# Optimization experiments

Measured on AMD Instinct MI355X. Metric: run time of the kernel, lower is better.

Reference implementation:

```python
import jax, jax.numpy as jnp
import numpy as np

DIM_IN = 512
HIDDEN = 512
DIM_OUT = 512
BATCH = 256

def _n_tri(d):
    return (d * d + d) // 2

def _quad_expand(x):
    # x: [B, D] -> [B, D + (D^2+D)/2] with upper-triu (incl diag) pairwise products
    d = x.shape[1]
    iu0, iu1 = np.triu_indices(d)  # static indices
    x_sq = x[:, iu0] * x[:, iu1]  # [B, n_tri] -- avoids materializing full outer
    return jnp.concatenate([x, x_sq], axis=-1)

def setup_inputs() -> dict:
    key = jax.random.key(0)
    k = jax.random.split(key, 5)
    f0 = DIM_IN + _n_tri(DIM_IN)
    f1 = HIDDEN + _n_tri(HIDDEN)
    s0 = 1.0 / np.sqrt(f0)
    s1 = 1.0 / np.sqrt(f1)
    return {
        "x": jax.random.normal(k[0], (BATCH, DIM_IN), dtype=jnp.float32),
        "W0": jax.random.uniform(k[1], (HIDDEN, f0), dtype=jnp.float32, minval=-s0, maxval=s0),
        "b0": jax.random.uniform(k[2], (HIDDEN,), dtype=jnp.float32, minval=-s0, maxval=s0),
        "W1": jax.random.uniform(k[3], (DIM_OUT, f1), dtype=jnp.float32, minval=-s1, maxval=s1),
        "b1": jax.random.uniform(k[4], (DIM_OUT,), dtype=jnp.float32, minval=-s1, maxval=s1),
    }

def reference(x, W0, b0, W1, b1):
    h = _quad_expand(x) @ W0.T + b0  # [B, HIDDEN]
    out = _quad_expand(h) @ W1.T + b1  # [B, DIM_OUT]
    return out
```

## Files before the change

kernel.cpp:

```cpp
#include <hip/hip_runtime.h>

typedef short s16x4 __attribute__((ext_vector_type(4)));
typedef short s16x8 __attribute__((ext_vector_type(8)));
typedef float f32x4 __attribute__((ext_vector_type(4)));

#define DIM     512
#define BATCH   256
#define NTRI    131328
#define FDIM    131840
#define KBLOCKS 2060
#define BN      64
#define NTILES  8
#define CMAX    128

__device__ __forceinline__ unsigned short f2bf(float f) {
  __bf16 h = (__bf16)f;
  return __builtin_bit_cast(unsigned short, h);
}
__device__ __forceinline__ float bf2f(unsigned short s) {
  union { unsigned u; float f; } v; v.u = (unsigned)s << 16; return v.f;
}
__device__ __forceinline__ int swz(int m) { return (m ^ (m >> 2)) & 7; }

__global__ void build_table(unsigned* __restrict__ table) {
  int i = blockIdx.x;
  int base = i * DIM - (i * (i - 1)) / 2;
  int len = DIM - i;
  for (int t = threadIdx.x; t < len; t += blockDim.x)
    table[base + t] = ((unsigned)i << 16) | (unsigned)(i + t);
}

__global__ void transpose_x(const float* __restrict__ x, unsigned short* __restrict__ Xt) {
  int t = blockIdx.x * blockDim.x + threadIdx.x;
  int r = t & (BATCH - 1);
  int c = t >> 8;
  Xt[c * BATCH + r] = f2bf(x[r * DIM + c]);
}

__global__ __launch_bounds__(512, 4)
void qgemm(const unsigned* __restrict__ table,
           const unsigned short* __restrict__ Xt,
           const float* __restrict__ W,
           float* __restrict__ partial,
           int C)
{
  __shared__ unsigned short As[BATCH * 64];
  __shared__ unsigned short Ws[64 * 64];
  const int ntile = blockIdx.x & (NTILES - 1);
  const int chunk = blockIdx.x >> 3;
  const int kb0 = (KBLOCKS * chunk) / C;
  const int kb1 = (KBLOCKS * (chunk + 1)) / C;
  const int n0 = ntile * BN;
  const int tid = threadIdx.x;
  const int lane = tid & 63;
  const int wave = tid >> 6;
  const int wm = wave & 3;
  const int wn = wave >> 2;
  const int lm = lane & 15;
  const int lk = lane >> 4;

  const int s8 = wave;
  const int m0 = lane * 4;
  const int wr0 = tid >> 4;
  const int wc16 = tid & 15;

  f32x4 acc[4][2] = {};

  for (int kb = kb0; kb < kb1; ++kb) {
    f32x4 wreg[2];
    #pragma unroll
    for (int it = 0; it < 2; ++it)
      wreg[it] = *(const f32x4*)(W + (size_t)(n0 + wr0 + it * 32) * FDIM + kb * 64 + wc16 * 4);

    {
      int f0 = kb * 64 + s8 * 8;
      unsigned w4[4][4];
      if (f0 < DIM) {
        s16x4 xj[8];
        #pragma unroll
        for (int e = 0; e < 8; ++e)
          xj[e] = *(const s16x4*)(Xt + (f0 + e) * BATCH + m0);
        #pragma unroll
        for (int ep = 0; ep < 4; ++ep)
          #pragma unroll
          for (int mm = 0; mm < 4; ++mm)
            w4[mm][ep] = (unsigned)(unsigned short)xj[2*ep][mm]
                       | ((unsigned)(unsigned short)xj[2*ep+1][mm] << 16);
      } else {
        int p0 = f0 - DIM;
        unsigned t0 = table[p0];
        unsigned t7 = table[p0 + 7];
        if ((t0 >> 16) == (t7 >> 16)) {
          int i = (int)(t0 >> 16), j0 = (int)(t0 & 0xffffu);
          s16x4 xi = *(const s16x4*)(Xt + i * BATCH + m0);
          s16x4 xj[8];
          #pragma unroll
          for (int e = 0; e < 8; ++e)
            xj[e] = *(const s16x4*)(Xt + (j0 + e) * BATCH + m0);
          float xif[4];
          #pragma unroll
          for (int mm = 0; mm < 4; ++mm) xif[mm] = bf2f((unsigned short)xi[mm]);
          #pragma unroll
          for (int ep = 0; ep < 4; ++ep)
            #pragma unroll
            for (int mm = 0; mm < 4; ++mm) {
              float a = xif[mm] * bf2f((unsigned short)xj[2*ep][mm]);
              float b = xif[mm] * bf2f((unsigned short)xj[2*ep+1][mm]);
              w4[mm][ep] = (unsigned)f2bf(a) | ((unsigned)f2bf(b) << 16);
            }
        } else {
          #pragma unroll
          for (int ep = 0; ep < 4; ++ep) {
            unsigned ta = table[p0 + 2*ep], tb = table[p0 + 2*ep + 1];
            s16x4 xia = *(const s16x4*)(Xt + (ta >> 16) * BATCH + m0);
            s16x4 xja = *(const s16x4*)(Xt + (ta & 0xffffu) * BATCH + m0);
            s16x4 xib = *(const s16x4*)(Xt + (tb >> 16) * BATCH + m0);
            s16x4 xjb = *(const s16x4*)(Xt + (tb & 0xffffu) * BATCH + m0);
            #pragma unroll
            for (int mm = 0; mm < 4; ++mm) {
              float a = bf2f((unsigned short)xia[mm]) * bf2f((unsigned short)xja[mm]);
              float b = bf2f((unsigned short)xib[mm]) * bf2f((unsigned short)xjb[mm]);
              w4[mm][ep] = (unsigned)f2bf(a) | ((unsigned)f2bf(b) << 16);
            }
          }
        }
      }
      #pragma unroll
      for (int mm = 0; mm < 4; ++mm) {
        int m = m0 + mm;
        int slot = s8 ^ swz(m);
        uint4 pk = make_uint4(w4[mm][0], w4[mm][1], w4[mm][2], w4[mm][3]);
        *(uint4*)((char*)As + m * 128 + slot * 16) = pk;
      }
    }

    #pragma unroll
    for (int it = 0; it < 2; ++it) {
      int r = wr0 + it * 32;
      unsigned lo = (unsigned)f2bf(wreg[it][0]) | ((unsigned)f2bf(wreg[it][1]) << 16);
      unsigned hi = (unsigned)f2bf(wreg[it][2]) | ((unsigned)f2bf(wreg[it][3]) << 16);
      int slot = (wc16 >> 1) ^ swz(r);
      *(uint2*)((char*)Ws + r * 128 + slot * 16 + (wc16 & 1) * 8) = make_uint2(lo, hi);
    }
    __syncthreads();

    #pragma unroll
    for (int ks = 0; ks < 2; ++ks) {
      s16x8 bfr[2], afr[4];
      #pragma unroll
      for (int nf = 0; nf < 2; ++nf) {
        int n = wn * 32 + nf * 16 + lm;
        int slot = (ks * 4 + lk) ^ swz(n);
        bfr[nf] = *(const s16x8*)((const char*)Ws + n * 128 + slot * 16);
      }
      #pragma unroll
      for (int mf = 0; mf < 4; ++mf) {
        int mm = wm * 64 + mf * 16 + lm;
        int slot = (ks * 4 + lk) ^ swz(mm);
        afr[mf] = *(const s16x8*)((const char*)As + mm * 128 + slot * 16);
      }
      #pragma unroll
      for (int mf = 0; mf < 4; ++mf)
        #pragma unroll
        for (int nf = 0; nf < 2; ++nf)
          acc[mf][nf] = __builtin_amdgcn_mfma_f32_16x16x32_bf16(afr[mf], bfr[nf], acc[mf][nf], 0, 0, 0);
    }
    __syncthreads();
  }

  float* pout = partial + (size_t)chunk * (BATCH * DIM);
  #pragma unroll
  for (int mf = 0; mf < 4; ++mf) {
    #pragma unroll
    for (int nf = 0; nf < 2; ++nf) {
      int mrow = wm * 64 + mf * 16 + lk * 4;
      int ncol = n0 + wn * 32 + nf * 16 + lm;
      #pragma unroll
      for (int r = 0; r < 4; ++r)
        pout[(size_t)(mrow + r) * DIM + ncol] = acc[mf][nf][r];
    }
  }
}

__global__ void reduce_h(const float* __restrict__ partial, const float* __restrict__ bias,
                         unsigned short* __restrict__ Ht, int C) {
  int t = blockIdx.x * blockDim.x + threadIdx.x;
  int b = t >> 9;
  int o = t & (DIM - 1);
  float s = bias[o];
  #pragma unroll 4
  for (int c = 0; c < C; ++c) s += partial[(size_t)c * (BATCH * DIM) + t];
  Ht[o * BATCH + b] = f2bf(s);
}

__global__ void reduce_out(const float* __restrict__ partial, const float* __restrict__ bias,
                           float* __restrict__ out, int C) {
  int t = blockIdx.x * blockDim.x + threadIdx.x;
  int o = t & (DIM - 1);
  float s = bias[o];
  #pragma unroll 4
  for (int c = 0; c < C; ++c) s += partial[(size_t)c * (BATCH * DIM) + t];
  out[t] = s;
}

extern "C" void kernel_launch(void* const* d_in, const int* in_sizes, int n_in,
                              void* d_out, int out_size, void* d_ws, size_t ws_size,
                              hipStream_t stream) {
  const float* x  = (const float*)d_in[0];
  const float* W0 = (const float*)d_in[1];
  const float* b0 = (const float*)d_in[2];
  const float* W1 = (const float*)d_in[3];
  const float* b1 = (const float*)d_in[4];
  float* out = (float*)d_out;

  char* ws = (char*)d_ws;
  unsigned* table    = (unsigned*)ws;
  unsigned short* Xt = (unsigned short*)(ws + 525312);
  unsigned short* Ht = (unsigned short*)(ws + 787456);
  float* partial     = (float*)(ws + 1049600);

  size_t avail = (ws_size > 1049600) ? (ws_size - 1049600) : 0;
  int C = (int)(avail / ((size_t)BATCH * DIM * sizeof(float)));
  if (C > CMAX) C = CMAX;
  if (C < 1)   C = 1;

  build_table<<<dim3(512), dim3(256), 0, stream>>>(table);
  transpose_x<<<dim3(512), dim3(256), 0, stream>>>(x, Xt);

  qgemm<<<dim3(NTILES * C), dim3(512), 0, stream>>>(table, Xt, W0, partial, C);
  reduce_h<<<dim3(512), dim3(256), 0, stream>>>(partial, b0, Ht, C);

  qgemm<<<dim3(NTILES * C), dim3(512), 0, stream>>>(table, Ht, W1, partial, C);
  reduce_out<<<dim3(512), dim3(256), 0, stream>>>(partial, b1, out, C);
}
```

Measured before the change: 255.0 us.

## Precompute quadratic feature tiles once and DMA them into LDS in GEMM

A new featgen kernel builds each 64-wide block of the quadratic feature matrix once, in bf16 and already in the swizzled LDS layout, and writes it to a large workspace buffer. The GEMM kernel then streams these tiles straight into shared memory with global_load_lds, rather than having all 8 N-tile blocks recompute the same products. W loads are also software-prefetched one k-block ahead, blocks are reordered so that adjacent blocks share an N tile, and the chunk count is lowered. The cost is about 67 MB of extra feature traffic per layer plus an extra launch, and it needs a larger workspace.

```diff
diff --git a/kernel.cpp b/kernel.cpp
--- a/kernel.cpp
+++ b/kernel.cpp
@@ -1,6 +1,5 @@
 #include <hip/hip_runtime.h>
 
-typedef short s16x4 __attribute__((ext_vector_type(4)));
 typedef short s16x8 __attribute__((ext_vector_type(8)));
 typedef float f32x4 __attribute__((ext_vector_type(4)));
 
@@ -11,7 +10,7 @@
 #define KBLOCKS 2060
 #define BN      64
 #define NTILES  8
-#define CMAX    128
+#define CCH     96
 
 __device__ __forceinline__ unsigned short f2bf(float f) {
   __bf16 h = (__bf16)f;
@@ -20,7 +19,16 @@
 __device__ __forceinline__ float bf2f(unsigned short s) {
   union { unsigned u; float f; } v; v.u = (unsigned)s << 16; return v.f;
 }
+__device__ __forceinline__ unsigned pk2(float a, float b) {
+  return (unsigned)f2bf(a) | ((unsigned)f2bf(b) << 16);
+}
 __device__ __forceinline__ int swz(int m) { return (m ^ (m >> 2)) & 7; }
+
+__device__ __forceinline__ void dma16(const void* g, void* l) {
+  __builtin_amdgcn_global_load_lds(
+      (const __attribute__((address_space(1))) void*)g,
+      (__attribute__((address_space(3))) void*)l, 16, 0, 0);
+}
 
 __global__ void build_table(unsigned* __restrict__ table) {
   int i = blockIdx.x;
@@ -37,17 +45,81 @@
   Xt[c * BATCH + r] = f2bf(x[r * DIM + c]);
 }
 
+__global__ __launch_bounds__(512)
+void featgen(const unsigned* __restrict__ table,
+             const unsigned short* __restrict__ Xt,
+             uint4* __restrict__ Feat)
+{
+  __shared__ uint4 img[2048];
+  const int kb = blockIdx.x;
+  const int tid = threadIdx.x;
+  const int s8 = tid >> 6;
+  const int lane = tid & 63;
+  const int f0 = kb * 64 + s8 * 8;
+
+  if (f0 < DIM) {
+    #pragma unroll
+    for (int mb = 0; mb < 4; ++mb) {
+      int m = mb * 64 + lane;
+      unsigned short v[8];
+      #pragma unroll
+      for (int e = 0; e < 8; ++e) v[e] = Xt[(f0 + e) * BATCH + m];
+      uint4 pk;
+      pk.x = (unsigned)v[0] | ((unsigned)v[1] << 16);
+      pk.y = (unsigned)v[2] | ((unsigned)v[3] << 16);
+      pk.z = (unsigned)v[4] | ((unsigned)v[5] << 16);
+      pk.w = (unsigned)v[6] | ((unsigned)v[7] << 16);
+      img[m * 8 + (s8 ^ swz(m))] = pk;
+    }
+  } else {
+    int p0 = f0 - DIM;
+    unsigned t0 = table[p0], t7 = table[p0 + 7];
+    if ((t0 >> 16) == (t7 >> 16)) {
+      int i = (int)(t0 >> 16), j0 = (int)(t0 & 0xffffu);
+      #pragma unroll
+      for (int mb = 0; mb < 4; ++mb) {
+        int m = mb * 64 + lane;
+        float xi = bf2f(Xt[i * BATCH + m]);
+        float pr[8];
+        #pragma unroll
+        for (int e = 0; e < 8; ++e) pr[e] = xi * bf2f(Xt[(j0 + e) * BATCH + m]);
+        uint4 pk = make_uint4(pk2(pr[0], pr[1]), pk2(pr[2], pr[3]),
+                              pk2(pr[4], pr[5]), pk2(pr[6], pr[7]));
+        img[m * 8 + (s8 ^ swz(m))] = pk;
+      }
+    } else {
+      unsigned tt[8];
+      #pragma unroll
+      for (int e = 0; e < 8; ++e) tt[e] = table[p0 + e];
+      #pragma unroll
+      for (int mb = 0; mb < 4; ++mb) {
+        int m = mb * 64 + lane;
+        float pr[8];
+        #pragma unroll
+        for (int e = 0; e < 8; ++e)
+          pr[e] = bf2f(Xt[(tt[e] >> 16) * BATCH + m]) * bf2f(Xt[(tt[e] & 0xffffu) * BATCH + m]);
+        uint4 pk = make_uint4(pk2(pr[0], pr[1]), pk2(pr[2], pr[3]),
+                              pk2(pr[4], pr[5]), pk2(pr[6], pr[7]));
+        img[m * 8 + (s8 ^ swz(m))] = pk;
+      }
+    }
+  }
+  __syncthreads();
+  uint4* out = Feat + (size_t)kb * 2048;
+  #pragma unroll
+  for (int p = 0; p < 4; ++p) out[p * 512 + tid] = img[p * 512 + tid];
+}
+
 __global__ __launch_bounds__(512, 4)
-void qgemm(const unsigned* __restrict__ table,
-           const unsigned short* __restrict__ Xt,
+void qgemm(const uint4* __restrict__ Feat,
            const float* __restrict__ W,
            float* __restrict__ partial,
            int C)
 {
   __shared__ unsigned short As[BATCH * 64];
   __shared__ unsigned short Ws[64 * 64];
-  const int ntile = blockIdx.x & (NTILES - 1);
-  const int chunk = blockIdx.x >> 3;
+  const int chunk = blockIdx.x % C;
+  const int ntile = blockIdx.x / C;
   const int kb0 = (KBLOCKS * chunk) / C;
   const int kb1 = (KBLOCKS * (chunk + 1)) / C;
   const int n0 = ntile * BN;
@@ -59,88 +131,35 @@
   const int lm = lane & 15;
   const int lk = lane >> 4;
 
-  const int s8 = wave;
-  const int m0 = lane * 4;
   const int wr0 = tid >> 4;
   const int wc16 = tid & 15;
 
   f32x4 acc[4][2] = {};
+  f32x4 wreg[2];
+
+  #pragma unroll
+  for (int it = 0; it < 2; ++it)
+    wreg[it] = *(const f32x4*)(W + (size_t)(n0 + wr0 + it * 32) * FDIM + kb0 * 64 + wc16 * 4);
+
+  const char* fsrc0 = (const char*)Feat + tid * 16;
+  char* adst = (char*)As + tid * 16;
 
   for (int kb = kb0; kb < kb1; ++kb) {
-    f32x4 wreg[2];
-    #pragma unroll
-    for (int it = 0; it < 2; ++it)
-      wreg[it] = *(const f32x4*)(W + (size_t)(n0 + wr0 + it * 32) * FDIM + kb * 64 + wc16 * 4);
-
-    {
-      int f0 = kb * 64 + s8 * 8;
-      unsigned w4[4][4];
-      if (f0 < DIM) {
-        s16x4 xj[8];
-        #pragma unroll
-        for (int e = 0; e < 8; ++e)
-          xj[e] = *(const s16x4*)(Xt + (f0 + e) * BATCH + m0);
-        #pragma unroll
-        for (int ep = 0; ep < 4; ++ep)
-          #pragma unroll
-          for (int mm = 0; mm < 4; ++mm)
-            w4[mm][ep] = (unsigned)(unsigned short)xj[2*ep][mm]
-                       | ((unsigned)(unsigned short)xj[2*ep+1][mm] << 16);
-      } else {
-        int p0 = f0 - DIM;
-        unsigned t0 = table[p0];
-        unsigned t7 = table[p0 + 7];
-        if ((t0 >> 16) == (t7 >> 16)) {
-          int i = (int)(t0 >> 16), j0 = (int)(t0 & 0xffffu);
-          s16x4 xi = *(const s16x4*)(Xt + i * BATCH + m0);
-          s16x4 xj[8];
-          #pragma unroll
-          for (int e = 0; e < 8; ++e)
-            xj[e] = *(const s16x4*)(Xt + (j0 + e) * BATCH + m0);
-          float xif[4];
-          #pragma unroll
-          for (int mm = 0; mm < 4; ++mm) xif[mm] = bf2f((unsigned short)xi[mm]);
-          #pragma unroll
-          for (int ep = 0; ep < 4; ++ep)
-            #pragma unroll
-            for (int mm = 0; mm < 4; ++mm) {
-              float a = xif[mm] * bf2f((unsigned short)xj[2*ep][mm]);
-              float b = xif[mm] * bf2f((unsigned short)xj[2*ep+1][mm]);
-              w4[mm][ep] = (unsigned)f2bf(a) | ((unsigned)f2bf(b) << 16);
-            }
-        } else {
-          #pragma unroll
-          for (int ep = 0; ep < 4; ++ep) {
-            unsigned ta = table[p0 + 2*ep], tb = table[p0 + 2*ep + 1];
-            s16x4 xia = *(const s16x4*)(Xt + (ta >> 16) * BATCH + m0);
-            s16x4 xja = *(const s16x4*)(Xt + (ta & 0xffffu) * BATCH + m0);
-            s16x4 xib = *(const s16x4*)(Xt + (tb >> 16) * BATCH + m0);
-            s16x4 xjb = *(const s16x4*)(Xt + (tb & 0xffffu) * BATCH + m0);
-            #pragma unroll
-            for (int mm = 0; mm < 4; ++mm) {
-              float a = bf2f((unsigned short)xia[mm]) * bf2f((unsigned short)xja[mm]);
-              float b = bf2f((unsigned short)xib[mm]) * bf2f((unsigned short)xjb[mm]);
-              w4[mm][ep] = (unsigned)f2bf(a) | ((unsigned)f2bf(b) << 16);
-            }
-          }
-        }
-      }
-      #pragma unroll
-      for (int mm = 0; mm < 4; ++mm) {
-        int m = m0 + mm;
-        int slot = s8 ^ swz(m);
-        uint4 pk = make_uint4(w4[mm][0], w4[mm][1], w4[mm][2], w4[mm][3]);
-        *(uint4*)((char*)As + m * 128 + slot * 16) = pk;
-      }
-    }
+    const char* src = fsrc0 + (size_t)kb * 32768;
+    #pragma unroll
+    for (int p = 0; p < 4; ++p) dma16(src + p * 8192, adst + p * 8192);
 
     #pragma unroll
     for (int it = 0; it < 2; ++it) {
       int r = wr0 + it * 32;
-      unsigned lo = (unsigned)f2bf(wreg[it][0]) | ((unsigned)f2bf(wreg[it][1]) << 16);
-      unsigned hi = (unsigned)f2bf(wreg[it][2]) | ((unsigned)f2bf(wreg[it][3]) << 16);
       int slot = (wc16 >> 1) ^ swz(r);
-      *(uint2*)((char*)Ws + r * 128 + slot * 16 + (wc16 & 1) * 8) = make_uint2(lo, hi);
+      *(uint2*)((char*)Ws + r * 128 + slot * 16 + (wc16 & 1) * 8) =
+          make_uint2(pk2(wreg[it][0], wreg[it][1]), pk2(wreg[it][2], wreg[it][3]));
+    }
+    if (kb + 1 < kb1) {
+      #pragma unroll
+      for (int it = 0; it < 2; ++it)
+        wreg[it] = *(const f32x4*)(W + (size_t)(n0 + wr0 + it * 32) * FDIM + (kb + 1) * 64 + wc16 * 4);
     }
     __syncthreads();
 
@@ -217,19 +236,23 @@
   unsigned* table    = (unsigned*)ws;
   unsigned short* Xt = (unsigned short*)(ws + 525312);
   unsigned short* Ht = (unsigned short*)(ws + 787456);
-  float* partial     = (float*)(ws + 1049600);
-
-  size_t avail = (ws_size > 1049600) ? (ws_size - 1049600) : 0;
+  uint4* Feat        = (uint4*)(ws + 1049600);
+  size_t feat_end    = 1049600 + (size_t)KBLOCKS * 32768;
+  float* partial     = (float*)(ws + feat_end);
+
+  size_t avail = (ws_size > feat_end) ? (ws_size - feat_end) : 0;
   int C = (int)(avail / ((size_t)BATCH * DIM * sizeof(float)));
-  if (C > CMAX) C = CMAX;
-  if (C < 1)   C = 1;
+  if (C > CCH) C = CCH;
+  if (C < 1)  C = 1;
 
   build_table<<<dim3(512), dim3(256), 0, stream>>>(table);
   transpose_x<<<dim3(512), dim3(256), 0, stream>>>(x, Xt);
 
-  qgemm<<<dim3(NTILES * C), dim3(512), 0, stream>>>(table, Xt, W0, partial, C);
+  featgen<<<dim3(KBLOCKS), dim3(512), 0, stream>>>(table, Xt, Feat);
+  qgemm<<<dim3(NTILES * C), dim3(512), 0, stream>>>(Feat, W0, partial, C);
   reduce_h<<<dim3(512), dim3(256), 0, stream>>>(partial, b0, Ht, C);
 
-  qgemm<<<dim3(NTILES * C), dim3(512), 0, stream>>>(table, Ht, W1, partial, C);
+  featgen<<<dim3(KBLOCKS), dim3(512), 0, stream>>>(table, Ht, Feat);
+  qgemm<<<dim3(NTILES * C), dim3(512), 0, stream>>>(Feat, W1, partial, C);
   reduce_out<<<dim3(512), dim3(256), 0, stream>>>(partial, b1, out, C);
 }
```

After: 249.4 us. 2.2% less time.
